# Optimization experiments

Hardware: AMD Instinct MI355X
Metric: run time of the kernel (lower is better)

## Reference

```python
import jax, jax.numpy as jnp
import numpy as np


def _bilinear_resample(inputs, offsets):
    # inputs: (b, s, s, c); offsets: (b, s, s, 2) -- faithful to tf_batch_map_offsets
    b, h, w, c = inputs.shape
    s = h  # square map assumed by original code (input_size = shape[1])
    n = h * w
    offs = offsets.reshape(b, n, 2)
    gi, gj = jnp.meshgrid(jnp.arange(s, dtype=inputs.dtype),
                          jnp.arange(s, dtype=inputs.dtype), indexing='ij')
    grid = jnp.stack([gi, gj], axis=-1).reshape(1, n, 2)
    coords = jnp.clip(offs + grid, 0.0, float(s - 1))  # (b, n, 2), [i, j]
    lt = jnp.floor(coords).astype(jnp.int32)  # (b, n, 2)
    rb = jnp.ceil(coords).astype(jnp.int32)
    bidx = jnp.arange(b)[:, None]  # (b, 1) broadcasts with (b, n) index maps

    def gather(ci, cj):
        return inputs[bidx, ci, cj]  # (b, n, c)

    vals_lt = gather(lt[..., 0], lt[..., 1])
    vals_rb = gather(rb[..., 0], rb[..., 1])
    vals_lb = gather(rb[..., 0], lt[..., 1])  # [ceil_i, floor_j]
    vals_rt = gather(lt[..., 0], rb[..., 1])  # [floor_i, ceil_j]

    frac = coords - lt.astype(coords.dtype)  # (b, n, 2) fractional offsets
    fy = frac[..., 1:2]  # column fraction (axis 1 of coords)
    fx = frac[..., 0:1]  # row fraction
    vals_t = vals_lt + (vals_rt - vals_lt) * fy
    vals_b = vals_lb + (vals_rb - vals_lb) * fy
    out = vals_t + (vals_b - vals_t) * fx  # (b, n, c)
    return out.reshape(b, h, w, c)


def setup_inputs() -> dict:
    key = jax.random.key(0)
    k1, k2 = jax.random.split(key)
    B, S, C = 16, 128, 128
    offsets = jax.random.normal(k1, (B, S, S, 2), dtype=jnp.float32)
    inputs = jax.random.normal(k2, (B, S, S, C), dtype=jnp.float32)
    return {"offsets": offsets, "inputs": inputs}


def reference(offsets, inputs):
    return _bilinear_resample(inputs, offsets)
```

## Files before the change

kernel.cpp:

```cpp
#include <hip/hip_runtime.h>


constexpr int S = 128;
constexpr int CVEC = 32;
constexpr int PIX_PER_BLOCK = 8;
constexpr int NXCD = 8;

typedef float f32x4 __attribute__((ext_vector_type(4)));

__global__ __launch_bounds__(256) void resample_kernel(
    const float2* __restrict__ offsets2,
    const float4* __restrict__ inputs4,
    float4* __restrict__ out4,
    int blocks_per_xcd)
{
    const int wg = (blockIdx.x % NXCD) * blocks_per_xcd + blockIdx.x / NXCD;

    const int tid    = threadIdx.x;
    const int lane_c = tid & 31;
    const int pix    = wg * PIX_PER_BLOCK + (tid >> 5);

    const int j   = pix & (S - 1);
    const int rem = pix >> 7;
    const int i   = rem & (S - 1);
    const int b   = rem >> 7;

    const float2 off = offsets2[pix];
    float y = fminf(fmaxf((float)i + off.x, 0.0f), (float)(S - 1));
    float x = fminf(fmaxf((float)j + off.y, 0.0f), (float)(S - 1));

    const float y0f = floorf(y);
    const float x0f = floorf(x);
    const int y0 = (int)y0f;
    const int x0 = (int)x0f;
    const int y1 = min(y0 + 1, S - 1);
    const int x1 = min(x0 + 1, S - 1);
    const float fy = y - y0f;
    const float fx = x - x0f;

    const int base = (b * S * S) * CVEC + lane_c;
    const int r0 = base + y0 * (S * CVEC);
    const int r1 = base + y1 * (S * CVEC);

    const float4 v00 = inputs4[r0 + x0 * CVEC];
    const float4 v01 = inputs4[r0 + x1 * CVEC];
    const float4 v10 = inputs4[r1 + x0 * CVEC];
    const float4 v11 = inputs4[r1 + x1 * CVEC];

    float4 vt, vb, o;
    vt.x = v00.x + (v01.x - v00.x) * fx;
    vt.y = v00.y + (v01.y - v00.y) * fx;
    vt.z = v00.z + (v01.z - v00.z) * fx;
    vt.w = v00.w + (v01.w - v00.w) * fx;
    vb.x = v10.x + (v11.x - v10.x) * fx;
    vb.y = v10.y + (v11.y - v10.y) * fx;
    vb.z = v10.z + (v11.z - v10.z) * fx;
    vb.w = v10.w + (v11.w - v10.w) * fx;
    o.x = vt.x + (vb.x - vt.x) * fy;
    o.y = vt.y + (vb.y - vt.y) * fy;
    o.z = vt.z + (vb.z - vt.z) * fy;
    o.w = vt.w + (vb.w - vt.w) * fy;

    union { float4 f4; f32x4 v; } u;
    u.f4 = o;
    __builtin_nontemporal_store(u.v, (f32x4*)&out4[(long long)pix * CVEC + lane_c]);
}

extern "C" void kernel_launch(void* const* d_in, const int* in_sizes, int n_in,
                              void* d_out, int out_size, void* d_ws, size_t ws_size,
                              hipStream_t stream) {
    const float2* offsets2 = (const float2*)d_in[0];
    const float4* inputs4  = (const float4*)d_in[1];
    float4*       out4     = (float4*)d_out;

    const int B = in_sizes[0] / (S * S * 2);
    const int total_pix = B * S * S;
    const int blocks = total_pix / PIX_PER_BLOCK;
    const int blocks_per_xcd = blocks / NXCD;

    resample_kernel<<<blocks, 256, 0, stream>>>(offsets2, inputs4, out4,
                                                blocks_per_xcd);
}
```

Baseline: 243.4 us.

## Process two pixels per thread and drop XCD block remapping

Each thread now handles two pixels eight apart instead of one. All eight gather loads are issued before any interpolation, so each wave has more memory requests in flight, and the grid shrinks by half. The XCD-aware block index remap is removed, so consecutive blocks are spread across XCDs by the default round-robin. That can change L2 locality for neighbouring taps that are shared between blocks.

```diff
diff --git a/kernel.cpp b/kernel.cpp
--- a/kernel.cpp
+++ b/kernel.cpp
@@ -3,29 +3,19 @@
 
 constexpr int S = 128;
 constexpr int CVEC = 32;
-constexpr int PIX_PER_BLOCK = 8;
-constexpr int NXCD = 8;
+constexpr int PIX_PER_BLOCK = 16;
 
 typedef float f32x4 __attribute__((ext_vector_type(4)));
 
-__global__ __launch_bounds__(256) void resample_kernel(
-    const float2* __restrict__ offsets2,
-    const float4* __restrict__ inputs4,
-    float4* __restrict__ out4,
-    int blocks_per_xcd)
+__device__ __forceinline__ void tap_setup(int pix, int lane_c, float2 off,
+                                          int& i00, int& i01, int& i10, int& i11,
+                                          float& fy, float& fx)
 {
-    const int wg = (blockIdx.x % NXCD) * blocks_per_xcd + blockIdx.x / NXCD;
-
-    const int tid    = threadIdx.x;
-    const int lane_c = tid & 31;
-    const int pix    = wg * PIX_PER_BLOCK + (tid >> 5);
-
     const int j   = pix & (S - 1);
     const int rem = pix >> 7;
     const int i   = rem & (S - 1);
     const int b   = rem >> 7;
 
-    const float2 off = offsets2[pix];
     float y = fminf(fmaxf((float)i + off.x, 0.0f), (float)(S - 1));
     float x = fminf(fmaxf((float)j + off.y, 0.0f), (float)(S - 1));
 
@@ -35,18 +25,22 @@
     const int x0 = (int)x0f;
     const int y1 = min(y0 + 1, S - 1);
     const int x1 = min(x0 + 1, S - 1);
-    const float fy = y - y0f;
-    const float fx = x - x0f;
+    fy = y - y0f;
+    fx = x - x0f;
 
     const int base = (b * S * S) * CVEC + lane_c;
     const int r0 = base + y0 * (S * CVEC);
     const int r1 = base + y1 * (S * CVEC);
+    i00 = r0 + x0 * CVEC;
+    i01 = r0 + x1 * CVEC;
+    i10 = r1 + x0 * CVEC;
+    i11 = r1 + x1 * CVEC;
+}
 
-    const float4 v00 = inputs4[r0 + x0 * CVEC];
-    const float4 v01 = inputs4[r0 + x1 * CVEC];
-    const float4 v10 = inputs4[r1 + x0 * CVEC];
-    const float4 v11 = inputs4[r1 + x1 * CVEC];
-
+__device__ __forceinline__ float4 bilerp(float4 v00, float4 v01,
+                                         float4 v10, float4 v11,
+                                         float fy, float fx)
+{
     float4 vt, vb, o;
     vt.x = v00.x + (v01.x - v00.x) * fx;
     vt.y = v00.y + (v01.y - v00.y) * fx;
@@ -60,10 +54,45 @@
     o.y = vt.y + (vb.y - vt.y) * fy;
     o.z = vt.z + (vb.z - vt.z) * fy;
     o.w = vt.w + (vb.w - vt.w) * fy;
+    return o;
+}
 
-    union { float4 f4; f32x4 v; } u;
-    u.f4 = o;
-    __builtin_nontemporal_store(u.v, (f32x4*)&out4[(long long)pix * CVEC + lane_c]);
+__global__ __launch_bounds__(256) void resample_kernel(
+    const float2* __restrict__ offsets2,
+    const float4* __restrict__ inputs4,
+    float4* __restrict__ out4)
+{
+    const int tid    = threadIdx.x;
+    const int lane_c = tid & 31;
+    const int pg     = tid >> 5;
+    const int pix0   = blockIdx.x * PIX_PER_BLOCK + pg;
+    const int pix1   = pix0 + 8;
+
+    const float2 off0 = offsets2[pix0];
+    const float2 off1 = offsets2[pix1];
+
+    int a00, a01, a10, a11; float fy0, fx0;
+    int b00, b01, b10, b11; float fy1, fx1;
+    tap_setup(pix0, lane_c, off0, a00, a01, a10, a11, fy0, fx0);
+    tap_setup(pix1, lane_c, off1, b00, b01, b10, b11, fy1, fx1);
+
+    const float4 va00 = inputs4[a00];
+    const float4 va01 = inputs4[a01];
+    const float4 va10 = inputs4[a10];
+    const float4 va11 = inputs4[a11];
+    const float4 vb00 = inputs4[b00];
+    const float4 vb01 = inputs4[b01];
+    const float4 vb10 = inputs4[b10];
+    const float4 vb11 = inputs4[b11];
+
+    const float4 o0 = bilerp(va00, va01, va10, va11, fy0, fx0);
+    const float4 o1 = bilerp(vb00, vb01, vb10, vb11, fy1, fx1);
+
+    union { float4 f4; f32x4 v; } u0, u1;
+    u0.f4 = o0;
+    u1.f4 = o1;
+    __builtin_nontemporal_store(u0.v, (f32x4*)&out4[(long long)pix0 * CVEC + lane_c]);
+    __builtin_nontemporal_store(u1.v, (f32x4*)&out4[(long long)pix1 * CVEC + lane_c]);
 }
 
 extern "C" void kernel_launch(void* const* d_in, const int* in_sizes, int n_in,
@@ -76,8 +105,6 @@
     const int B = in_sizes[0] / (S * S * 2);
     const int total_pix = B * S * S;
     const int blocks = total_pix / PIX_PER_BLOCK;
-    const int blocks_per_xcd = blocks / NXCD;
 
-    resample_kernel<<<blocks, 256, 0, stream>>>(offsets2, inputs4, out4,
-                                                blocks_per_xcd);
+    resample_kernel<<<blocks, 256, 0, stream>>>(offsets2, inputs4, out4);
 }
```

Measured after the change: 233.7 us. -4.0%, faster.

## Stage haloed input tiles in shared memory per channel slice for bilinear gathers

Applied to the files above, without the earlier changes.

Each 512-thread block now owns a 16x32 pixel tile and a 16-channel slice. It loads a haloed input window (3-pixel margin) into LDS, then does the four-tap bilinear gathers from LDS, with a global-memory fallback for samples whose taps fall outside the window. The goal is to replace scattered global gathers, which read each input pixel about four times, with one coalesced window load per tile. The cost is redundant halo loads, a block-wide barrier, and a divergent global fallback for large offsets. The old XCD-aware block remapping is dropped, and the grid is indexed by slice, tile and batch instead.

```diff
diff --git a/kernel.cpp b/kernel.cpp
--- a/kernel.cpp
+++ b/kernel.cpp
@@ -1,52 +1,21 @@
 #include <hip/hip_runtime.h>
 
 
-constexpr int S = 128;
-constexpr int CVEC = 32;
-constexpr int PIX_PER_BLOCK = 8;
-constexpr int NXCD = 8;
+constexpr int S  = 128;
+constexpr int TR = 16;
+constexpr int TC = 32;
+constexpr int G  = 3;
+constexpr int WR = TR + 2 * G + 1;
+constexpr int WC = TC + 2 * G + 1;
+constexpr int PXW = WR * WC;
+constexpr int PX_STRIDE_F4 = 5;
 
 typedef float f32x4 __attribute__((ext_vector_type(4)));
 
-__global__ __launch_bounds__(256) void resample_kernel(
-    const float2* __restrict__ offsets2,
-    const float4* __restrict__ inputs4,
-    float4* __restrict__ out4,
-    int blocks_per_xcd)
+__device__ __forceinline__ float4 bilerp(float4 v00, float4 v01,
+                                         float4 v10, float4 v11,
+                                         float fy, float fx)
 {
-    const int wg = (blockIdx.x % NXCD) * blocks_per_xcd + blockIdx.x / NXCD;
-
-    const int tid    = threadIdx.x;
-    const int lane_c = tid & 31;
-    const int pix    = wg * PIX_PER_BLOCK + (tid >> 5);
-
-    const int j   = pix & (S - 1);
-    const int rem = pix >> 7;
-    const int i   = rem & (S - 1);
-    const int b   = rem >> 7;
-
-    const float2 off = offsets2[pix];
-    float y = fminf(fmaxf((float)i + off.x, 0.0f), (float)(S - 1));
-    float x = fminf(fmaxf((float)j + off.y, 0.0f), (float)(S - 1));
-
-    const float y0f = floorf(y);
-    const float x0f = floorf(x);
-    const int y0 = (int)y0f;
-    const int x0 = (int)x0f;
-    const int y1 = min(y0 + 1, S - 1);
-    const int x1 = min(x0 + 1, S - 1);
-    const float fy = y - y0f;
-    const float fx = x - x0f;
-
-    const int base = (b * S * S) * CVEC + lane_c;
-    const int r0 = base + y0 * (S * CVEC);
-    const int r1 = base + y1 * (S * CVEC);
-
-    const float4 v00 = inputs4[r0 + x0 * CVEC];
-    const float4 v01 = inputs4[r0 + x1 * CVEC];
-    const float4 v10 = inputs4[r1 + x0 * CVEC];
-    const float4 v11 = inputs4[r1 + x1 * CVEC];
-
     float4 vt, vb, o;
     vt.x = v00.x + (v01.x - v00.x) * fx;
     vt.y = v00.y + (v01.y - v00.y) * fx;
@@ -60,10 +29,104 @@
     o.y = vt.y + (vb.y - vt.y) * fy;
     o.z = vt.z + (vb.z - vt.z) * fy;
     o.w = vt.w + (vb.w - vt.w) * fy;
+    return o;
+}
 
-    union { float4 f4; f32x4 v; } u;
-    u.f4 = o;
-    __builtin_nontemporal_store(u.v, (f32x4*)&out4[(long long)pix * CVEC + lane_c]);
+__device__ __forceinline__ void nt_store(float4* dst, float4 v)
+{
+    union { float4 f4; f32x4 x; } u;
+    u.f4 = v;
+    __builtin_nontemporal_store(u.x, (f32x4*)dst);
+}
+
+__global__ __launch_bounds__(512) void resample_kernel(
+    const float2* __restrict__ offsets2,
+    const float4* __restrict__ inputs4,
+    float4* __restrict__ out4)
+{
+    __shared__ float4 smem[PXW * PX_STRIDE_F4];
+
+    const int tid   = threadIdx.x;
+    const int bid   = blockIdx.x;
+    const int slice = bid & 7;
+    const int tile  = (bid >> 3) & 31;
+    const int b     = bid >> 8;
+    const int t0    = (tile >> 2) * TR;
+    const int j0    = (tile & 3) * TC;
+    const int cbase = slice << 2;
+
+    const int wr0 = t0 - G;
+    const int wc0 = j0 - G;
+
+    #pragma unroll
+    for (int k = 0; k < 8; ++k) {
+        const int f = tid + (k << 9);
+        if (f < PXW * 4) {
+            const int p  = f >> 2;
+            const int q  = f & 3;
+            const int wy = p / WC;
+            const int wx = p - wy * WC;
+            const int gy = min(max(wr0 + wy, 0), S - 1);
+            const int gx = min(max(wc0 + wx, 0), S - 1);
+            smem[p * PX_STRIDE_F4 + q] =
+                inputs4[((((b << 7) | gy) << 7) | gx) * 32 + cbase + q];
+        }
+    }
+
+    const int prow = tid >> 5;
+    const int pcol = tid & 31;
+    const int row  = t0 + prow;
+    const int col  = j0 + pcol;
+    const int pix  = (((b << 7) | row) << 7) | col;
+    const float2 off = offsets2[pix];
+
+    float y = fminf(fmaxf((float)row + off.x, 0.0f), (float)(S - 1));
+    float x = fminf(fmaxf((float)col + off.y, 0.0f), (float)(S - 1));
+    const float y0f = floorf(y);
+    const float x0f = floorf(x);
+    const int y0 = (int)y0f;
+    const int x0 = (int)x0f;
+    const int y1 = min(y0 + 1, S - 1);
+    const int x1 = min(x0 + 1, S - 1);
+    const float fy = y - y0f;
+    const float fx = x - x0f;
+
+    __syncthreads();
+
+    const int outbase = pix * 32 + cbase;
+    const bool inwin = (y0 >= wr0) & (y1 <= wr0 + WR - 1) &
+                       (x0 >= wc0) & (x1 <= wc0 + WC - 1);
+
+    if (inwin) {
+        const int sb  = (y0 - wr0) * WC + (x0 - wc0);
+        const int dX  = x1 - x0;
+        const int dY  = (y1 - y0) * WC;
+        const int t00 = sb * PX_STRIDE_F4;
+        const int t01 = (sb + dX) * PX_STRIDE_F4;
+        const int t10 = (sb + dY) * PX_STRIDE_F4;
+        const int t11 = (sb + dY + dX) * PX_STRIDE_F4;
+        #pragma unroll
+        for (int q = 0; q < 4; ++q) {
+            const float4 v00 = smem[t00 + q];
+            const float4 v01 = smem[t01 + q];
+            const float4 v10 = smem[t10 + q];
+            const float4 v11 = smem[t11 + q];
+            nt_store(&out4[outbase + q], bilerp(v00, v01, v10, v11, fy, fx));
+        }
+    } else {
+        const int r00 = ((((b << 7) | y0) << 7) | x0) * 32 + cbase;
+        const int r01 = ((((b << 7) | y0) << 7) | x1) * 32 + cbase;
+        const int r10 = ((((b << 7) | y1) << 7) | x0) * 32 + cbase;
+        const int r11 = ((((b << 7) | y1) << 7) | x1) * 32 + cbase;
+        #pragma unroll
+        for (int q = 0; q < 4; ++q) {
+            const float4 v00 = inputs4[r00 + q];
+            const float4 v01 = inputs4[r01 + q];
+            const float4 v10 = inputs4[r10 + q];
+            const float4 v11 = inputs4[r11 + q];
+            nt_store(&out4[outbase + q], bilerp(v00, v01, v10, v11, fy, fx));
+        }
+    }
 }
 
 extern "C" void kernel_launch(void* const* d_in, const int* in_sizes, int n_in,
@@ -74,10 +137,7 @@
     float4*       out4     = (float4*)d_out;
 
     const int B = in_sizes[0] / (S * S * 2);
-    const int total_pix = B * S * S;
-    const int blocks = total_pix / PIX_PER_BLOCK;
-    const int blocks_per_xcd = blocks / NXCD;
+    const int blocks = B * 32 * 8;
 
-    resample_kernel<<<blocks, 256, 0, stream>>>(offsets2, inputs4, out4,
-                                                blocks_per_xcd);
+    resample_kernel<<<blocks, 512, 0, stream>>>(offsets2, inputs4, out4);
 }
```

After: 415.9 us. 70.9% more time.
